# Kernel tuning notes

Measured on AMD Instinct MI355X. Metric: run time of the kernel, lower is better.

The kernel has to match this reference:

```python
import jax, jax.numpy as jnp
import numpy as np

EPS = 1e-5

def batchnorm(x, g, b):
    # training-mode BN over (B, H, W) per channel, biased variance (PyTorch normalization)
    m = jnp.mean(x, axis=(0, 2, 3), keepdims=True)
    v = jnp.var(x, axis=(0, 2, 3), keepdims=True)
    return (x - m) * jax.lax.rsqrt(v + EPS) * g[None, :, None, None] + b[None, :, None, None]

def softmax_one(x, axis):
    # exp(x - max) / (1 + sum exp(x - max))  -- 'quiet softmax' used by PAConv ScoreNet
    x = x - jnp.max(x, axis=axis, keepdims=True)
    e = jnp.exp(x)
    return e / (1.0 + jnp.sum(e, axis=axis, keepdims=True))

def setup_inputs() -> dict:
    key = jax.random.key(0)
    ks = jax.random.split(key, 6)
    B, N, k, Cin, Cout, M = 4, 4096, 32, 64, 64, 8
    return {
        "grouped_xyz": jax.random.normal(ks[0], (B, 3, N, k), jnp.float32),
        "feature": jax.random.normal(ks[1], (B, Cin, N, k), jnp.float32),
        "w1": jax.random.normal(ks[2], (16, 4), jnp.float32) * 0.5,        # ScoreNet conv1 (1x1, no bias)
        "g1": jnp.ones((16,), jnp.float32),
        "b1": jnp.zeros((16,), jnp.float32),
        "w2": jax.random.normal(ks[3], (M, 16), jnp.float32) * 0.25,       # ScoreNet conv2 (1x1, bias)
        "b2": jnp.zeros((M,), jnp.float32),
        "weightbank": jax.random.normal(ks[4], (Cin, M * Cout), jnp.float32) * (2.0 / Cin) ** 0.5,
        "g_out": jnp.ones((Cout,), jnp.float32),
        "b_out": jnp.zeros((Cout,), jnp.float32),
    }

def reference(grouped_xyz, feature, w1, g1, b1, w2, b2, weightbank, g_out, b_out):
    B, _, N, k = grouped_xyz.shape
    M = w2.shape[0]
    # distance channel
    xyz_ed = jnp.linalg.norm(grouped_xyz, axis=1, keepdims=True)          # (B,1,N,k)
    xyz = jnp.concatenate([grouped_xyz, xyz_ed], axis=1)                  # (B,4,N,k)
    # ScoreNet: conv1x1 -> BN -> ReLU -> conv1x1(+bias) -> softmax_one
    h = jax.nn.relu(batchnorm(jnp.einsum('oc,bcnk->bonk', w1, xyz), g1, b1))
    s = jnp.einsum('oc,bcnk->bonk', w2, h) + b2[None, :, None, None]       # (B,M,N,k)
    scores = softmax_one(s, axis=1).transpose(0, 2, 3, 1)                  # (B,N,k,M)
    # weightbank projection + score-weighted combine
    feat = feature.transpose(0, 2, 3, 1)                                   # (B,N,k,Cin)
    proj = jnp.matmul(feat, weightbank).reshape(B, N, k, M, -1)            # (B,N,k,M,Cout)
    out = jnp.einsum('bnkm,bnkmc->bnkc', scores, proj).transpose(0, 3, 1, 2)  # (B,Cout,N,k)
    out = batchnorm(out, g_out, b_out)
    return jax.nn.relu(out)
```

## Files before the change

### kernel.cpp

```cpp
#include <hip/hip_runtime.h>
#include <hip/hip_bf16.h>
#include <math.h>

#define PB 4
#define PN 4096
#define PK 32
#define NKP (PN * PK)
#define PTOT (PB * NKP)
#define CIN 64
#define COUT 64
#define PM 8
#define HID 16
#define EPS 1e-5f

#define WS_MOM 0
#define WS_A2 288
#define WS_PSUM 416
#define WS_PSQ 2464
#define WS_ZERO_FLOATS 4512
#define WS_WBT 4608

typedef __attribute__((ext_vector_type(8))) short short8;
typedef __attribute__((ext_vector_type(4))) float float4v;
typedef __attribute__((ext_vector_type(4))) unsigned int uint4v;
typedef unsigned int uint32;
typedef unsigned short ushort16;

static __device__ __forceinline__ ushort16 f2bf(float v) {
  uint32 u = __builtin_bit_cast(uint32, v);
  return (ushort16)((u + 0x8000u) >> 16);
}

static __device__ __forceinline__ void gload_lds16(const float* g, float* l) {
  __builtin_amdgcn_global_load_lds(
      (const __attribute__((address_space(1))) void*)g,
      (__attribute__((address_space(3))) void*)l, 16, 0, 0);
}

#define MOMB 256
__global__ __launch_bounds__(256) void k_pre(const float* __restrict__ gx,
                                             const float* __restrict__ wb,
                                             float* __restrict__ ws) {
  if (blockIdx.x >= MOMB) {
    int idx = (int)(blockIdx.x - MOMB) * 256 + threadIdx.x;
    int ci = idx >> 9;
    int col = idx & 511;
    ((ushort16*)(ws + WS_WBT))[col * 64 + ci] = f2bf(wb[idx]);
    return;
  }
  float s[14];
#pragma unroll
  for (int i = 0; i < 14; ++i) s[i] = 0.f;
  int tid = blockIdx.x * 256 + threadIdx.x;
  const int nth = MOMB * 256;
  for (int p = tid; p < PTOT; p += nth) {
    int b = p >> 17;
    int r = p & (NKP - 1);
    const float* base = gx + (size_t)b * 3 * NKP + r;
    float v[4];
    v[0] = base[0];
    v[1] = base[NKP];
    v[2] = base[2 * NKP];
    v[3] = sqrtf(v[0] * v[0] + v[1] * v[1] + v[2] * v[2]);
#pragma unroll
    for (int j = 0; j < 4; ++j) s[j] += v[j];
    int idx = 4;
#pragma unroll
    for (int j = 0; j < 4; ++j)
#pragma unroll
      for (int l = j; l < 4; ++l) s[idx++] += v[j] * v[l];
  }
#pragma unroll
  for (int i = 0; i < 14; ++i) {
    float x = s[i];
#pragma unroll
    for (int off = 32; off > 0; off >>= 1) x += __shfl_down(x, off, 64);
    s[i] = x;
  }
  __shared__ float red[4][14];
  int wave = threadIdx.x >> 6;
  if ((threadIdx.x & 63) == 0) {
#pragma unroll
    for (int i = 0; i < 14; ++i) red[wave][i] = s[i];
  }
  __syncthreads();
  if (threadIdx.x < 14) {
    float v = red[0][threadIdx.x] + red[1][threadIdx.x] +
              red[2][threadIdx.x] + red[3][threadIdx.x];
    atomicAdd(&ws[WS_MOM + threadIdx.x * 16], v);
  }
}

#define PPB 512
#define SUB 64
#define SM_SCL 8192

__global__ __launch_bounds__(256, 3) void k_main_mfma(
    const float* __restrict__ gx, const float* __restrict__ feat,
    const float* __restrict__ w1, const float* __restrict__ g1,
    const float* __restrict__ b1, const float* __restrict__ w2,
    const float* __restrict__ b2, const ushort16* __restrict__ wbt,
    float* __restrict__ ws, float* __restrict__ out) {
  __shared__ float smem[12288];

  const int t = threadIdx.x;
  const int pblk = blockIdx.x * PPB;
  const int b = pblk >> 17;
  const int r0 = pblk & (NKP - 1);
  const int w = t >> 6;
  const int L = t & 63;
  const int l16 = L & 15;
  const int q4 = L >> 4;
  const int wchan = w * 16;

  float a1r[HID], b1r[HID];
  {
    const float invP = 1.f / (float)PTOT;
    float mu[4], S[4][4];
#pragma unroll
    for (int j = 0; j < 4; ++j) mu[j] = ws[WS_MOM + j * 16] * invP;
    int idx = 4;
#pragma unroll
    for (int j = 0; j < 4; ++j)
#pragma unroll
      for (int l = j; l < 4; ++l) {
        float v = ws[WS_MOM + idx * 16] * invP;
        ++idx;
        S[j][l] = v;
        S[l][j] = v;
      }
#pragma unroll
    for (int c = 0; c < HID; ++c) {
      float wv[4];
#pragma unroll
      for (int j = 0; j < 4; ++j) wv[j] = w1[c * 4 + j];
      float mean = 0.f;
#pragma unroll
      for (int j = 0; j < 4; ++j) mean += wv[j] * mu[j];
      float Et2 = 0.f;
#pragma unroll
      for (int j = 0; j < 4; ++j)
#pragma unroll
        for (int l = 0; l < 4; ++l) Et2 += wv[j] * wv[l] * S[j][l];
      float var = Et2 - mean * mean;
      float a = g1[c] * rsqrtf(var + EPS);
      a1r[c] = a;
      b1r[c] = b1[c] - a * mean;
    }
  }

  uint4v bwu[PM][2];
#pragma unroll
  for (int m = 0; m < PM; ++m)
#pragma unroll
    for (int ks = 0; ks < 2; ++ks)
      bwu[m][ks] = *(const uint4v*)(wbt + (m * 64 + wchan + l16) * 64 +
                                    ks * 32 + q4 * 8);
#pragma unroll
  for (int m = 0; m < PM; ++m)
    asm volatile("" : "+v"(bwu[m][0]), "+v"(bwu[m][1]));

  float px[2], py[2], pz[2];
  {
    const float* gb = gx + (size_t)b * 3 * NKP + r0;
#pragma unroll
    for (int pp = 0; pp < 2; ++pp) {
      int p = t + pp * 256;
      px[pp] = gb[p];
      py[pp] = gb[NKP + p];
      pz[pp] = gb[2 * NKP + p];
    }
  }

  const float* fb = feat + (size_t)b * CIN * NKP + r0;
  auto STAGE = [&](int s) {
    float* dst = &smem[(s & 1) * 4096];
    const float* src = fb + s * SUB;
#pragma unroll
    for (int i = 0; i < 4; ++i) {
      int chunk = w * 4 + i;
      int ci = chunk * 4 + q4;
      int sp = (l16 << 2) ^ (((ci >> 3) & 1) << 4);
      gload_lds16(src + (size_t)ci * NKP + sp, dst + chunk * 256);
    }
  };

  STAGE(0);
  STAGE(1);
  __builtin_amdgcn_sched_barrier(0);

#pragma unroll
  for (int pp = 0; pp < 2; ++pp) {
    float x = px[pp], y = py[pp], z = pz[pp];
    float ed = sqrtf(x * x + y * y + z * z);
    float h[HID];
#pragma unroll
    for (int c = 0; c < HID; ++c) {
      float tv = w1[c * 4 + 0] * x + w1[c * 4 + 1] * y + w1[c * 4 + 2] * z +
                 w1[c * 4 + 3] * ed;
      h[c] = fmaxf(a1r[c] * tv + b1r[c], 0.f);
    }
    float sc[PM];
#pragma unroll
    for (int m = 0; m < PM; ++m) {
      float a = b2[m];
#pragma unroll
      for (int c = 0; c < HID; ++c) a += w2[m * HID + c] * h[c];
      sc[m] = a;
    }
    float mx = sc[0];
#pragma unroll
    for (int m = 1; m < PM; ++m) mx = fmaxf(mx, sc[m]);
    float esum = 0.f;
#pragma unroll
    for (int m = 0; m < PM; ++m) {
      sc[m] = __expf(sc[m] - mx);
      esum += sc[m];
    }
    float inv = 1.f / (1.f + esum);
    int p = t + pp * 256;
#pragma unroll
    for (int m = 0; m < PM; ++m) smem[SM_SCL + m * 512 + p] = sc[m] * inv;
  }

  float sacc[4] = {0.f, 0.f, 0.f, 0.f};
  float qacc[4] = {0.f, 0.f, 0.f, 0.f};
  float* ob = out + (size_t)b * COUT * NKP + r0;

  auto COMPUTE = [&](int s) {
    const float* bufp = &smem[(s & 1) * 4096];
    uint4v ffb[4][2];
#pragma unroll
    for (int rt = 0; rt < 4; ++rt) {
      int p = rt * 16 + l16;
#pragma unroll
      for (int ks = 0; ks < 2; ++ks) {
        int cib = ks * 32 + q4 * 8;
        int psw = p ^ (((cib >> 3) & 1) << 4);
        const float* cp = bufp + cib * 64 + psw;
#pragma unroll
        for (int e = 0; e < 4; ++e) {
          uint32 u0 = __builtin_bit_cast(uint32, cp[(2 * e) * 64]) + 0x8000u;
          uint32 u1 =
              __builtin_bit_cast(uint32, cp[(2 * e + 1) * 64]) + 0x8000u;
          ffb[rt][ks][e] = __builtin_amdgcn_perm(u1, u0, 0x07060302u);
        }
      }
    }
    float4v fin[4];
#pragma unroll
    for (int rt = 0; rt < 4; ++rt) fin[rt] = (float4v)0.f;
#pragma unroll
    for (int m = 0; m < PM; ++m) {
      float sm[4];
#pragma unroll
      for (int rt = 0; rt < 4; ++rt)
        sm[rt] = smem[SM_SCL + m * 512 + s * SUB + rt * 16 + l16];
#pragma unroll
      for (int rt = 0; rt < 4; ++rt) {
        float4v g = (float4v)0.f;
        g = __builtin_amdgcn_mfma_f32_16x16x32_bf16(
            __builtin_bit_cast(short8, bwu[m][0]),
            __builtin_bit_cast(short8, ffb[rt][0]), g, 0, 0, 0);
        g = __builtin_amdgcn_mfma_f32_16x16x32_bf16(
            __builtin_bit_cast(short8, bwu[m][1]),
            __builtin_bit_cast(short8, ffb[rt][1]), g, 0, 0, 0);
#pragma unroll
        for (int r = 0; r < 4; ++r) fin[rt][r] += sm[rt] * g[r];
      }
    }
    __builtin_amdgcn_sched_barrier(0);
#pragma unroll
    for (int rt = 0; rt < 4; ++rt) {
      int p = s * SUB + rt * 16 + l16;
#pragma unroll
      for (int r = 0; r < 4; ++r) {
        float v = fin[rt][r];
        ob[(size_t)(wchan + q4 * 4 + r) * NKP + p] = v;
        sacc[r] += v;
        qacc[r] += v * v;
      }
    }
  };

#define ENTRY(VM_STR)                                       \
  asm volatile("s_waitcnt vmcnt(" VM_STR ")" ::: "memory"); \
  __builtin_amdgcn_s_barrier();                             \
  __builtin_amdgcn_sched_barrier(0);

#define EXITB()                      \
  __builtin_amdgcn_sched_barrier(0); \
  __builtin_amdgcn_s_barrier();      \
  __builtin_amdgcn_sched_barrier(0);

  asm volatile("s_waitcnt vmcnt(4) lgkmcnt(0)" ::: "memory");
  __builtin_amdgcn_s_barrier();
  __builtin_amdgcn_sched_barrier(0);
  COMPUTE(0);
  EXITB();
  STAGE(2);
  __builtin_amdgcn_sched_barrier(0);

  ENTRY("20") COMPUTE(1); EXITB(); STAGE(3); __builtin_amdgcn_sched_barrier(0);
  ENTRY("20") COMPUTE(2); EXITB(); STAGE(4); __builtin_amdgcn_sched_barrier(0);
  ENTRY("20") COMPUTE(3); EXITB(); STAGE(5); __builtin_amdgcn_sched_barrier(0);
  ENTRY("20") COMPUTE(4); EXITB(); STAGE(6); __builtin_amdgcn_sched_barrier(0);
  ENTRY("20") COMPUTE(5); EXITB(); STAGE(7); __builtin_amdgcn_sched_barrier(0);
  ENTRY("20") COMPUTE(6); EXITB();
  ENTRY("16") COMPUTE(7);

#undef ENTRY
#undef EXITB

#pragma unroll
  for (int off = 1; off < 16; off <<= 1) {
#pragma unroll
    for (int r = 0; r < 4; ++r) {
      sacc[r] += __shfl_xor(sacc[r], off, 64);
      qacc[r] += __shfl_xor(qacc[r], off, 64);
    }
  }
  if (l16 == 0) {
    int slot = blockIdx.x & 31;
#pragma unroll
    for (int r = 0; r < 4; ++r) {
      atomicAdd(&ws[WS_PSUM + slot * 64 + wchan + q4 * 4 + r], sacc[r]);
      atomicAdd(&ws[WS_PSQ + slot * 64 + wchan + q4 * 4 + r], qacc[r]);
    }
  }
}

#define NORMB 4096
__global__ __launch_bounds__(256) void k_norm(float* __restrict__ out,
                                              const float* __restrict__ ws,
                                              const float* __restrict__ g_out,
                                              const float* __restrict__ b_out) {
  __shared__ float a2s[COUT], b2s[COUT];
  const int t = threadIdx.x;
  if (t < COUT) {
    float s = 0.f, q = 0.f;
#pragma unroll
    for (int sl = 0; sl < 32; ++sl) {
      s += ws[WS_PSUM + sl * 64 + t];
      q += ws[WS_PSQ + sl * 64 + t];
    }
    const float invP = 1.f / (float)PTOT;
    float mean = s * invP;
    float var = q * invP - mean * mean;
    float a = g_out[t] * rsqrtf(var + EPS);
    a2s[t] = a;
    b2s[t] = b_out[t] - a * mean;
  }
  __syncthreads();
  size_t i4 = (size_t)blockIdx.x * 256 + t;
  const size_t stride = (size_t)NORMB * 256;
  float4* p = (float4*)out;
#pragma unroll
  for (int it = 0; it < 8; ++it, i4 += stride) {
    int c = (int)((i4 >> 15) & 63);
    float a = a2s[c];
    float bb = b2s[c];
    float4 v = p[i4];
    v.x = fmaxf(a * v.x + bb, 0.f);
    v.y = fmaxf(a * v.y + bb, 0.f);
    v.z = fmaxf(a * v.z + bb, 0.f);
    v.w = fmaxf(a * v.w + bb, 0.f);
    p[i4] = v;
  }
}

extern "C" void kernel_launch(void* const* d_in, const int* in_sizes, int n_in,
                              void* d_out, int out_size, void* d_ws,
                              size_t ws_size, hipStream_t stream) {
  const float* gx = (const float*)d_in[0];
  const float* feat = (const float*)d_in[1];
  const float* w1 = (const float*)d_in[2];
  const float* g1 = (const float*)d_in[3];
  const float* b1 = (const float*)d_in[4];
  const float* w2 = (const float*)d_in[5];
  const float* b2 = (const float*)d_in[6];
  const float* wb = (const float*)d_in[7];
  const float* g_out = (const float*)d_in[8];
  const float* b_out = (const float*)d_in[9];
  float* out = (float*)d_out;
  float* ws = (float*)d_ws;
  ushort16* wbt = (ushort16*)(ws + WS_WBT);

  (void)in_sizes; (void)n_in; (void)out_size; (void)ws_size;

  hipMemsetAsync(d_ws, 0, WS_ZERO_FLOATS * sizeof(float), stream);

  k_pre<<<MOMB + 128, 256, 0, stream>>>(gx, wb, ws);
  k_main_mfma<<<PTOT / PPB, 256, 0, stream>>>(gx, feat, w1, g1, b1, w2, b2,
                                              wbt, ws, out);
  k_norm<<<NORMB, 256, 0, stream>>>(out, ws, g_out, b_out);
}
```

Before: 347.0 us.

## Transpose MFMA operands for vectorized output stores and swizzled score layout

Swaps the MFMA A/B operands so each lane holds four consecutive points of one output channel. This allows 16-byte vector stores to the output instead of scalar strided stores. Scores are stored point-major with an XOR swizzle so each point's 8 scores load as two float4 reads, and the BN partial-stat reduction shrinks to two shuffles. The first pass now reads xyz with float4 loads. The extra rt-loop restructure changes register pressure and the vmcnt wait counts, which depend on the exact number of issued loads per stage.

```diff
diff --git a/kernel.cpp b/kernel.cpp
--- a/kernel.cpp
+++ b/kernel.cpp
@@ -14,7 +14,6 @@
 #define EPS 1e-5f
 
 #define WS_MOM 0
-#define WS_A2 288
 #define WS_PSUM 416
 #define WS_PSQ 2464
 #define WS_ZERO_FLOATS 4512
@@ -35,6 +34,10 @@
   __builtin_amdgcn_global_load_lds(
       (const __attribute__((address_space(1))) void*)g,
       (__attribute__((address_space(3))) void*)l, 16, 0, 0);
+}
+
+static __device__ __forceinline__ int scl_addr(int p) {
+  return (p * 8) ^ (((p >> 2) & 3) << 3);
 }
 
 #define MOMB 256
@@ -53,22 +56,28 @@
   for (int i = 0; i < 14; ++i) s[i] = 0.f;
   int tid = blockIdx.x * 256 + threadIdx.x;
   const int nth = MOMB * 256;
-  for (int p = tid; p < PTOT; p += nth) {
-    int b = p >> 17;
-    int r = p & (NKP - 1);
+  for (int p4 = tid * 4; p4 < PTOT; p4 += nth * 4) {
+    int b = p4 >> 17;
+    int r = p4 & (NKP - 1);
     const float* base = gx + (size_t)b * 3 * NKP + r;
-    float v[4];
-    v[0] = base[0];
-    v[1] = base[NKP];
-    v[2] = base[2 * NKP];
-    v[3] = sqrtf(v[0] * v[0] + v[1] * v[1] + v[2] * v[2]);
-#pragma unroll
-    for (int j = 0; j < 4; ++j) s[j] += v[j];
-    int idx = 4;
-#pragma unroll
-    for (int j = 0; j < 4; ++j)
-#pragma unroll
-      for (int l = j; l < 4; ++l) s[idx++] += v[j] * v[l];
+    float4v xv = *(const float4v*)(base);
+    float4v yv = *(const float4v*)(base + NKP);
+    float4v zv = *(const float4v*)(base + 2 * NKP);
+#pragma unroll
+    for (int j = 0; j < 4; ++j) {
+      float v[4];
+      v[0] = xv[j];
+      v[1] = yv[j];
+      v[2] = zv[j];
+      v[3] = sqrtf(v[0] * v[0] + v[1] * v[1] + v[2] * v[2]);
+#pragma unroll
+      for (int q = 0; q < 4; ++q) s[q] += v[q];
+      int idx = 4;
+#pragma unroll
+      for (int q = 0; q < 4; ++q)
+#pragma unroll
+        for (int l = q; l < 4; ++l) s[idx++] += v[q] * v[l];
+    }
   }
 #pragma unroll
   for (int i = 0; i < 14; ++i) {
@@ -219,67 +228,68 @@
     }
     float inv = 1.f / (1.f + esum);
     int p = t + pp * 256;
-#pragma unroll
-    for (int m = 0; m < PM; ++m) smem[SM_SCL + m * 512 + p] = sc[m] * inv;
-  }
-
-  float sacc[4] = {0.f, 0.f, 0.f, 0.f};
-  float qacc[4] = {0.f, 0.f, 0.f, 0.f};
-  float* ob = out + (size_t)b * COUT * NKP + r0;
+    int sa = scl_addr(p);
+    float4v v0, v1;
+#pragma unroll
+    for (int m = 0; m < 4; ++m) v0[m] = sc[m] * inv;
+#pragma unroll
+    for (int m = 0; m < 4; ++m) v1[m] = sc[4 + m] * inv;
+    *(float4v*)&smem[SM_SCL + sa] = v0;
+    *(float4v*)&smem[SM_SCL + sa + 4] = v1;
+  }
+
+  float sacc = 0.f, qacc = 0.f;
+  float* obl = out + (size_t)b * COUT * NKP + (size_t)(wchan + l16) * NKP + r0 +
+               q4 * 4;
 
   auto COMPUTE = [&](int s) {
     const float* bufp = &smem[(s & 1) * 4096];
-    uint4v ffb[4][2];
 #pragma unroll
     for (int rt = 0; rt < 4; ++rt) {
-      int p = rt * 16 + l16;
+      uint4v ffb[2];
 #pragma unroll
       for (int ks = 0; ks < 2; ++ks) {
         int cib = ks * 32 + q4 * 8;
-        int psw = p ^ (((cib >> 3) & 1) << 4);
+        int psw = (rt * 16 + l16) ^ (((cib >> 3) & 1) << 4);
         const float* cp = bufp + cib * 64 + psw;
 #pragma unroll
         for (int e = 0; e < 4; ++e) {
           uint32 u0 = __builtin_bit_cast(uint32, cp[(2 * e) * 64]) + 0x8000u;
           uint32 u1 =
               __builtin_bit_cast(uint32, cp[(2 * e + 1) * 64]) + 0x8000u;
-          ffb[rt][ks][e] = __builtin_amdgcn_perm(u1, u0, 0x07060302u);
+          ffb[ks][e] = __builtin_amdgcn_perm(u1, u0, 0x07060302u);
         }
       }
-    }
-    float4v fin[4];
-#pragma unroll
-    for (int rt = 0; rt < 4; ++rt) fin[rt] = (float4v)0.f;
-#pragma unroll
-    for (int m = 0; m < PM; ++m) {
-      float sm[4];
-#pragma unroll
-      for (int rt = 0; rt < 4; ++rt)
-        sm[rt] = smem[SM_SCL + m * 512 + s * SUB + rt * 16 + l16];
-#pragma unroll
-      for (int rt = 0; rt < 4; ++rt) {
-        float4v g = (float4v)0.f;
-        g = __builtin_amdgcn_mfma_f32_16x16x32_bf16(
-            __builtin_bit_cast(short8, bwu[m][0]),
-            __builtin_bit_cast(short8, ffb[rt][0]), g, 0, 0, 0);
-        g = __builtin_amdgcn_mfma_f32_16x16x32_bf16(
-            __builtin_bit_cast(short8, bwu[m][1]),
-            __builtin_bit_cast(short8, ffb[rt][1]), g, 0, 0, 0);
-#pragma unroll
-        for (int r = 0; r < 4; ++r) fin[rt][r] += sm[rt] * g[r];
+      float4v g[PM];
+#pragma unroll
+      for (int m = 0; m < PM; ++m) {
+        float4v z = (float4v)0.f;
+        z = __builtin_amdgcn_mfma_f32_16x16x32_bf16(
+            __builtin_bit_cast(short8, ffb[0]),
+            __builtin_bit_cast(short8, bwu[m][0]), z, 0, 0, 0);
+        g[m] = __builtin_amdgcn_mfma_f32_16x16x32_bf16(
+            __builtin_bit_cast(short8, ffb[1]),
+            __builtin_bit_cast(short8, bwu[m][1]), z, 0, 0, 0);
       }
-    }
-    __builtin_amdgcn_sched_barrier(0);
-#pragma unroll
-    for (int rt = 0; rt < 4; ++rt) {
-      int p = s * SUB + rt * 16 + l16;
+      float4v fin;
 #pragma unroll
       for (int r = 0; r < 4; ++r) {
-        float v = fin[rt][r];
-        ob[(size_t)(wchan + q4 * 4 + r) * NKP + p] = v;
-        sacc[r] += v;
-        qacc[r] += v * v;
+        int pr = s * SUB + rt * 16 + q4 * 4 + r;
+        int sa = scl_addr(pr);
+        float4v s0 = *(const float4v*)&smem[SM_SCL + sa];
+        float4v s1 = *(const float4v*)&smem[SM_SCL + sa + 4];
+        float a = 0.f;
+#pragma unroll
+        for (int m = 0; m < 4; ++m) a += s0[m] * g[m][r];
+#pragma unroll
+        for (int m = 0; m < 4; ++m) a += s1[m] * g[4 + m][r];
+        fin[r] = a;
+        sacc += a;
+        qacc += a * a;
       }
+      __builtin_amdgcn_sched_barrier(0);
+      *(float4v*)(obl + s * SUB + rt * 16) = fin;
+      __builtin_amdgcn_sched_barrier(0);
     }
   };
 
@@ -301,32 +311,25 @@
   STAGE(2);
   __builtin_amdgcn_sched_barrier(0);
 
-  ENTRY("20") COMPUTE(1); EXITB(); STAGE(3); __builtin_amdgcn_sched_barrier(0);
-  ENTRY("20") COMPUTE(2); EXITB(); STAGE(4); __builtin_amdgcn_sched_barrier(0);
-  ENTRY("20") COMPUTE(3); EXITB(); STAGE(5); __builtin_amdgcn_sched_barrier(0);
-  ENTRY("20") COMPUTE(4); EXITB(); STAGE(6); __builtin_amdgcn_sched_barrier(0);
-  ENTRY("20") COMPUTE(5); EXITB(); STAGE(7); __builtin_amdgcn_sched_barrier(0);
-  ENTRY("20") COMPUTE(6); EXITB();
-  ENTRY("16") COMPUTE(7);
+  ENTRY("8") COMPUTE(1); EXITB(); STAGE(3); __builtin_amdgcn_sched_barrier(0);
+  ENTRY("8") COMPUTE(2); EXITB(); STAGE(4); __builtin_amdgcn_sched_barrier(0);
+  ENTRY("8") COMPUTE(3); EXITB(); STAGE(5); __builtin_amdgcn_sched_barrier(0);
+  ENTRY("8") COMPUTE(4); EXITB(); STAGE(6); __builtin_amdgcn_sched_barrier(0);
+  ENTRY("8") COMPUTE(5); EXITB(); STAGE(7); __builtin_amdgcn_sched_barrier(0);
+  ENTRY("8") COMPUTE(6); EXITB();
+  ENTRY("4") COMPUTE(7);
 
 #undef ENTRY
 #undef EXITB
 
-#pragma unroll
-  for (int off = 1; off < 16; off <<= 1) {
-#pragma unroll
-    for (int r = 0; r < 4; ++r) {
-      sacc[r] += __shfl_xor(sacc[r], off, 64);
-      qacc[r] += __shfl_xor(qacc[r], off, 64);
-    }
-  }
-  if (l16 == 0) {
+  sacc += __shfl_xor(sacc, 16, 64);
+  qacc += __shfl_xor(qacc, 16, 64);
+  sacc += __shfl_xor(sacc, 32, 64);
+  qacc += __shfl_xor(qacc, 32, 64);
+  if (L < 16) {
     int slot = blockIdx.x & 31;
-#pragma unroll
-    for (int r = 0; r < 4; ++r) {
-      atomicAdd(&ws[WS_PSUM + slot * 64 + wchan + q4 * 4 + r], sacc[r]);
-      atomicAdd(&ws[WS_PSQ + slot * 64 + wchan + q4 * 4 + r], qacc[r]);
-    }
+    atomicAdd(&ws[WS_PSUM + slot * 64 + wchan + l16], sacc);
+    atomicAdd(&ws[WS_PSQ + slot * 64 + wchan + l16], qacc);
   }
 }
 
```

Result: no change. 341.1 us (-1.7%).
